# Performance work log

Hardware: AMD Instinct MI355X
Metric: run time of the kernel (lower is better)

## Reference

```python
import jax, jax.numpy as jnp
import numpy as np

H = 4          # attention heads
K = 16         # knn neighbors
EPS = 1e-5     # BatchNorm eps


def setup_inputs() -> dict:
    key = jax.random.key(0)
    ks = jax.random.split(key, 10)
    B, C, T, N = 2, 128, 32, 512
    OUT = 128
    HID = 2 * C + 2 * OUT  # ff hidden = in*2 + out*2
    s = 0.02
    return {
        "x_all": jax.random.normal(ks[0], (B, C, T, N), jnp.float32),
        "Wq": jax.random.normal(ks[1], (C, C), jnp.float32) * s,
        "Wk": jax.random.normal(ks[2], (C, C), jnp.float32) * s,
        "Wv": jax.random.normal(ks[3], (C, C), jnp.float32) * s,
        "W1": jax.random.normal(ks[4], (HID, C), jnp.float32) * s,
        "W2": jax.random.normal(ks[5], (OUT, HID), jnp.float32) * s,
        "bn_gamma": 1.0 + 0.1 * jax.random.normal(ks[6], (OUT,), jnp.float32),
        "bn_beta": 0.1 * jax.random.normal(ks[7], (OUT,), jnp.float32),
        "bn_mean": 0.1 * jax.random.normal(ks[8], (OUT,), jnp.float32),
        "bn_var": jax.random.uniform(ks[9], (OUT,), jnp.float32, 0.5, 1.5),
    }


def reference(x_all, Wq, Wk, Wv, W1, W2, bn_gamma, bn_beta, bn_mean, bn_var):
    B, C, T, N = x_all.shape
    D = C // H
    # --- st_group_points: candidate pool = 3 consecutive frames (replicate temporal pad), frame-major ---
    xp = jnp.concatenate([x_all[:, :, :1], x_all, x_all[:, :, -1:]], axis=2)   # (B,C,T+2,N)
    pool = jnp.stack([xp[:, :, :-2], xp[:, :, 1:-1], xp[:, :, 2:]], axis=3)    # (B,C,T,3,N)
    pool = pool.reshape(B, C, T, 3 * N)                                        # (B,C,T,3N)
    # KNN on xyz (channels 0:3); sqrt is monotone so topk on squared dists gives same indices
    a = x_all[:, :3]                                                           # (B,3,T,N)
    b = pool[:, :3]                                                            # (B,3,T,3N)
    d2 = jnp.sum((a[..., :, None] - b[..., None, :]) ** 2, axis=1)             # (B,T,N,3N)
    _, idx = jax.lax.top_k(-d2, K)                                             # (B,T,N,K) smallest-dist
    nb = jnp.take_along_axis(pool[:, :, :, None, :], idx[:, None], axis=-1)    # (B,C,T,N,K)
    rel = x_all[..., None] - nb                                                # diff grouping (B,C,T,N,K)
    # --- per-point local attention over K neighbors (1x1 convs == channel matmuls), all t at once ---
    q = jnp.einsum('oc,bctn->botn', Wq, x_all).reshape(B, H, D, T, N)
    k = jnp.einsum('oc,bctnk->botnk', Wk, rel).reshape(B, H, D, T, N, K)
    v = jnp.einsum('oc,bctnk->botnk', Wv, rel).reshape(B, H, D, T, N, K)
    energy = jnp.einsum('bhdtn,bhdtnk->bhtnk', q, k) / jnp.sqrt(jnp.float32(D))
    attn = jax.nn.softmax(energy, axis=-1)                                     # (B,H,T,N,K)
    agg = jnp.einsum('bhtnk,bhdtnk->bhdtn', attn, v).reshape(B, C, T, N)
    # --- residual + BatchNorm1d (eval mode, running stats) + conv feed-forward ---
    h = x_all + agg
    scale = (bn_gamma / jnp.sqrt(bn_var + EPS))[None, :, None, None]
    h = (h - bn_mean[None, :, None, None]) * scale + bn_beta[None, :, None, None]
    h = jax.nn.leaky_relu(jnp.einsum('oc,bctn->botn', W1, h), 0.2)
    y = jnp.einsum('oc,bctn->botn', W2, h)                                     # (B,OUT,T,N)
    return jnp.concatenate([x_all[:, :4], y], axis=1)                          # (B,4+OUT,T,N)
```

## Files before the change

kernel.cpp:

```cpp
#include <hip/hip_runtime.h>
#include <hip/hip_bf16.h>

typedef __hip_bfloat16 bf16;
typedef unsigned long long u64;
typedef __attribute__((ext_vector_type(8))) short short8;
typedef __attribute__((ext_vector_type(4))) float f32x4;

#define B_   2
#define C_   128
#define T_   32
#define N_   512
#define K_   16
#define HID_ 512
#define TN   (T_*N_)
#define PTS  (B_*T_*N_)

#define MFMA_BF16(a,b,c) __builtin_amdgcn_mfma_f32_16x16x32_bf16((a),(b),(c),0,0,0)

__device__ __forceinline__ float b2f(bf16 v){ return __bfloat162float(v); }
__device__ __forceinline__ bf16  f2b(float v){ return __float2bfloat16(v); }

__device__ __forceinline__ float ldc(const void* p, int i, bool f32) {
  return f32 ? ((const float*)p)[i] : b2f(((const bf16*)p)[i]);
}

__global__ __launch_bounds__(256) void convw_kernel(
    const void* __restrict__ x,
    const void* wq, const void* wk, const void* wv,
    const void* w1, const void* w2, const void* g, const void* bb,
    const void* m, const void* v,
    bf16* __restrict__ wqb, bf16* __restrict__ wkb, bf16* __restrict__ wvb,
    bf16* __restrict__ w1b, bf16* __restrict__ w2b,
    float* __restrict__ gf, float* __restrict__ bf_, float* __restrict__ mf,
    float* __restrict__ vf, int* __restrict__ flag)
{
  __shared__ int cnt;
  if (threadIdx.x == 0) cnt = 0;
  __syncthreads();
  const unsigned short* u = (const unsigned short*)x;
  int w = 0;
#pragma unroll
  for (int j = 0; j < 8; ++j) {
    unsigned short hv = u[threadIdx.x*8 + j];
    int e = (hv >> 7) & 0xFF;
    if (e >= 0x89) w++;
  }
  if (w) atomicAdd(&cnt, w);
  __syncthreads();
  bool f32 = (cnt > 32);
  if (blockIdx.x == 0 && threadIdx.x == 0) *flag = f32 ? 1 : 0;

  int i = blockIdx.x*256 + threadIdx.x;
  if (i < 16384) { wqb[i] = f2b(ldc(wq, i, f32)); return; } i -= 16384;
  if (i < 16384) { wkb[i] = f2b(ldc(wk, i, f32)); return; } i -= 16384;
  if (i < 16384) { wvb[i] = f2b(ldc(wv, i, f32)); return; } i -= 16384;
  if (i < 65536) { w1b[i] = f2b(ldc(w1, i, f32)); return; } i -= 65536;
  if (i < 65536) { w2b[i] = f2b(ldc(w2, i, f32)); return; } i -= 65536;
  if (i < 128)   { gf[i]  = ldc(g, i, f32); return; }       i -= 128;
  if (i < 128)   { bf_[i] = ldc(bb, i, f32); return; }      i -= 128;
  if (i < 128)   { mf[i]  = ldc(m, i, f32); return; }       i -= 128;
  if (i < 128)   { vf[i]  = ldc(v, i, f32); return; }
}

__device__ __forceinline__ void proj_gemm(const bf16* __restrict__ W,
                                          bf16 (*ys)[136],
                                          const short8 am[4][4],
                                          int mrow, int quad, int wave)
{
#pragma unroll
  for (int oi = 0; oi < 2; ++oi) {
    int ot = wave*2 + oi;
    f32x4 acc[4];
#pragma unroll
    for (int mt=0;mt<4;++mt) acc[mt] = (f32x4){0.f,0.f,0.f,0.f};
#pragma unroll
    for (int kq=0;kq<4;++kq) {
      short8 bfr = *(const short8*)&W[(ot*16+mrow)*C_ + kq*32 + quad*8];
#pragma unroll
      for (int mt=0;mt<4;++mt) acc[mt] = MFMA_BF16(am[mt][kq], bfr, acc[mt]);
    }
#pragma unroll
    for (int mt=0;mt<4;++mt)
#pragma unroll
      for (int r=0;r<4;++r)
        ys[mt*16 + quad*4 + r][ot*16 + mrow] = f2b(acc[mt][r]);
  }
}

__device__ __forceinline__ void tile_store128(bf16* __restrict__ dst,
                                              const bf16 (*ys)[136], int tid)
{
#pragma unroll
  for (int it=0; it<4; ++it) {
    int flat = (it*256 + tid)*8;
    int p = flat >> 7, c = flat & 127;
    *(short8*)&dst[(size_t)p*C_ + c] = *(const short8*)&ys[p][c];
  }
}

__global__ __launch_bounds__(256) void proj_kernel(
    const void* __restrict__ x, const int* __restrict__ flag,
    const bf16* __restrict__ wqb, const bf16* __restrict__ wkb, const bf16* __restrict__ wvb,
    bf16* __restrict__ xTb, bf16* QT, bf16* __restrict__ KT, bf16* __restrict__ VT)
{
  __shared__ bf16 xs [64][136];
  __shared__ bf16 ysK[64][136];
  __shared__ bf16 ysV[64][136];
  int tid = threadIdx.x;
  int p0  = blockIdx.x * 64;
  int b   = p0 >> 14; int tn0 = p0 & (TN-1);
  if (*flag) {
    const float* xbase = (const float*)x + (size_t)b*C_*TN + tn0;
#pragma unroll
    for (int it=0; it<32; ++it) {
      int i = it*256 + tid;
      int c = i >> 6, p = i & 63;
      xs[p][c] = f2b(xbase[(size_t)c*TN + p]);
    }
  } else {
    const bf16* xbase = (const bf16*)x + (size_t)b*C_*TN + tn0;
#pragma unroll
    for (int it=0; it<32; ++it) {
      int i = it*256 + tid;
      int c = i >> 6, p = i & 63;
      xs[p][c] = xbase[(size_t)c*TN + p];
    }
  }
  __syncthreads();
  tile_store128(xTb + (size_t)p0*C_, xs, tid);
  int lane = tid & 63, wave = tid >> 6;
  int mrow = lane & 15, quad = lane >> 4;
  short8 am[4][4];
#pragma unroll
  for (int mt=0;mt<4;++mt)
#pragma unroll
    for (int kq=0;kq<4;++kq)
      am[mt][kq] = *(const short8*)&xs[mt*16 + mrow][kq*32 + quad*8];
  __syncthreads();
  proj_gemm(wqb, xs,  am, mrow, quad, wave);
  proj_gemm(wkb, ysK, am, mrow, quad, wave);
  proj_gemm(wvb, ysV, am, mrow, quad, wave);
  __syncthreads();
  tile_store128(QT + (size_t)p0*C_, xs,  tid);
  tile_store128(KT + (size_t)p0*C_, ysK, tid);
  tile_store128(VT + (size_t)p0*C_, ysV, tid);
}

__device__ __forceinline__ u64 shflx64(u64 v, int m) {
  return (u64)__shfl_xor((long long)v, m, 64);
}
template<int W>
__device__ __forceinline__ u64 bitonic64w(u64 key, int lane) {
#pragma unroll
  for (int k = 2; k <= W; k <<= 1) {
#pragma unroll
    for (int j = k >> 1; j >= 1; j >>= 1) {
      u64 p = shflx64(key, j);
      bool keep_min = ((lane & k) == 0) == ((lane & j) == 0);
      key = ((p < key) == keep_min) ? p : key;
    }
  }
  return key;
}
__device__ __forceinline__ unsigned bitonic32u(unsigned key, int lane) {
#pragma unroll
  for (int k = 2; k <= 64; k <<= 1) {
#pragma unroll
    for (int j = k >> 1; j >= 1; j >>= 1) {
      unsigned p = (unsigned)__shfl_xor((int)key, j, 64);
      bool keep_min = ((lane & k) == 0) == ((lane & j) == 0);
      key = ((p < key) == keep_min) ? p : key;
    }
  }
  return key;
}

__global__ __launch_bounds__(512) void knn_kernel(const void* __restrict__ x,
                                                  const int* __restrict__ flag,
                                                  int* __restrict__ idxout)
{
  __shared__ float4 cand4[3*N_];
  __shared__ u64 surv[8][64];
  int tid = threadIdx.x;
  int blk = blockIdx.x;
  int row = blk >> 6;
  int b = row >> 5, t = row & 31;
  int ng = blk & 63;
  bool f32 = (*flag != 0);
#pragma unroll
  for (int q = 0; q < 3; ++q) {
    int tt = t - 1 + q; tt = tt < 0 ? 0 : (tt > T_-1 ? T_-1 : tt);
    size_t base = ((size_t)b*C_*T_ + tt)*(size_t)N_ + tid;
    float c0, c1, c2;
    if (f32) {
      const float* xp = (const float*)x;
      c0 = xp[base]; c1 = xp[base + (size_t)T_*N_]; c2 = xp[base + 2*(size_t)T_*N_];
    } else {
      const bf16* xp = (const bf16*)x;
      c0 = b2f(xp[base]); c1 = b2f(xp[base + (size_t)T_*N_]); c2 = b2f(xp[base + 2*(size_t)T_*N_]);
    }
    cand4[q*N_ + tid] = make_float4(c0, c1, c2, 0.f);
  }
  __syncthreads();
  int wave = tid >> 6, lane = tid & 63;
  int n = ng*8 + wave;
  float4 a = cand4[N_ + n];
  unsigned db[24];
#pragma unroll
  for (int j = 0; j < 24; ++j) {
    float4 cm = cand4[lane + (j << 6)];
    float dx = a.x - cm.x;
    float dy = a.y - cm.y;
    float dz = a.z - cm.z;
    float d2 = __fadd_rn(__fadd_rn(__fmul_rn(dx,dx), __fmul_rn(dy,dy)), __fmul_rn(dz,dz));
    db[j] = __float_as_uint(d2);
  }
  unsigned bd = db[0];
#pragma unroll
  for (int j = 1; j < 24; ++j) bd = (db[j] < bd) ? db[j] : bd;
  unsigned sd = bitonic32u(bd, lane);
  unsigned U = (unsigned)__shfl((int)sd, 15, 64);
  int c = 0;
#pragma unroll
  for (int j = 0; j < 24; ++j) c += (db[j] <= U) ? 1 : 0;
  int sc = c;
#pragma unroll
  for (int d = 1; d < 64; d <<= 1) {
    int pv = __shfl_up(sc, d, 64);
    if (lane >= d) sc += pv;
  }
  int total = __shfl(sc, 63, 64);
  int ofs = sc - c;
  u64 out16;
  if (total <= 64) {
#pragma unroll
    for (int j = 0; j < 24; ++j) {
      if (db[j] <= U) {
        surv[wave][ofs] = ((u64)db[j] << 32) | (unsigned)(lane + (j << 6));
        ++ofs;
      }
    }
    __threadfence_block();
    u64 kk = (lane < total) ? surv[wave][lane] : ~0ull;
    out16 = (total <= 32) ? bitonic64w<32>(kk, lane)
                          : bitonic64w<64>(kk, lane);
  } else {
    u64 key[24];
#pragma unroll
    for (int j = 0; j < 24; ++j)
      key[j] = ((u64)db[j] << 32) | (unsigned)(lane + (j << 6));
    u64 res = ~0ull;
#pragma unroll 1
    for (int r = 0; r < 16; ++r) {
      u64 m2 = key[0];
#pragma unroll
      for (int j = 1; j < 24; ++j) m2 = (key[j] < m2) ? key[j] : m2;
#pragma unroll
      for (int s = 32; s >= 1; s >>= 1) {
        u64 p = shflx64(m2, s);
        m2 = (p < m2) ? p : m2;
      }
      if (lane == r) res = m2;
      int mwin = (int)(m2 & 0xffffffffu);
      int sel = ((mwin & 63) == lane) ? (mwin >> 6) : -1;
#pragma unroll
      for (int j = 0; j < 24; ++j) if (j == sel) key[j] = ~0ull;
    }
    out16 = res;
  }
  int point = (b*T_ + t)*N_ + n;
  if (lane < K_) idxout[point*K_ + lane] = (int)(out16 & 0xffffffffu);
}

__global__ __launch_bounds__(512) void attn_kernel(
    const int* __restrict__ idxin, const bf16* __restrict__ xTb,
    bf16* qhT , const bf16* __restrict__ KT,
    const bf16* __restrict__ VT,
    const float* __restrict__ gf, const float* __restrict__ bf_,
    const float* __restrict__ mf, const float* __restrict__ vf)
{
  __shared__ int   col_lds[4][16];
  __shared__ float qbuf[4][C_];
  __shared__ bf16  kbuf[4][K_][136];
  __shared__ bf16  vbuf[4][K_][136];
  __shared__ float e_lds[4][4][16];
  int tid = threadIdx.x;
  int pt = tid >> 7, o = tid & 127;
  int point = blockIdx.x*4 + pt;
  int b = point >> 14; int tn = point & (TN-1); int t = tn >> 9;
  if (o < K_) {
    int m = idxin[point*K_ + o];
    int j = m >> 9, nn = m & (N_-1);
    int tt = t-1+j; tt = tt<0?0:(tt>T_-1?T_-1:tt);
    col_lds[pt][o] = ((b*T_ + tt)*N_ + nn)*C_;
  }
  int self = point*C_;
  qbuf[pt][o] = b2f(qhT[self + o]);
  __syncthreads();
#pragma unroll
  for (int it = 0; it < 2; ++it) {
    int i = it*512 + tid;
    int pp = i >> 8, rem = i & 255, k = rem >> 4, ch = rem & 15;
    int src = col_lds[pp][k] + ch*8;
    *(short8*)&kbuf[pp][k][ch*8] = *(const short8*)&KT[src];
    *(short8*)&vbuf[pp][k][ch*8] = *(const short8*)&VT[src];
  }
  __syncthreads();
  if (tid < 256) {
    int pp = tid >> 6, j = tid & 63, hd = j >> 4, k = j & 15;
    const float* qp = &qbuf[pp][hd*32];
    const bf16*  kp = &kbuf[pp][k][hd*32];
    float e = 0.f;
#pragma unroll
    for (int d=0; d<32; ++d) e = fmaf(qp[d], b2f(kp[d]), e);
    e_lds[pp][hd][k] = -e * 0.17677669529663687f;
  }
  __syncthreads();
  int hd = o >> 5;
  float e[16]; float mx = -3e38f;
#pragma unroll
  for (int k=0;k<K_;++k){ e[k]=e_lds[pt][hd][k]; mx=fmaxf(mx,e[k]); }
  float ssum=0.f;
#pragma unroll
  for (int k=0;k<K_;++k){ e[k]=__expf(e[k]-mx); ssum+=e[k]; }
  float inv = 1.f/ssum;
  float acc = b2f(VT[self + o]);
#pragma unroll
  for (int k=0;k<K_;++k)
    acc = fmaf(-(e[k]*inv), b2f(vbuf[pt][k][o]), acc);
  float hv = b2f(xTb[self + o]) + acc;
  float sc = gf[o] / sqrtf(vf[o] + 1e-5f);
  qhT[self + o] = f2b((hv - mf[o])*sc + bf_[o]);
}

__global__ __launch_bounds__(256) void mlp_kernel(const bf16* __restrict__ hT,
                                                  const bf16* __restrict__ w1b,
                                                  const bf16* __restrict__ w2b,
                                                  const void* __restrict__ x,
                                                  const int* __restrict__ flag,
                                                  void* out)
{
  __shared__ bf16 hidh[32][264];
  int tid = threadIdx.x;
  int p0 = blockIdx.x*32;
  int lane = tid & 63, wave = tid >> 6;
  int mrow = lane & 15, quad = lane >> 4;
  bool f32o = (*flag != 0);
  int bb = p0 >> 14;
  int tn0 = p0 & (TN-1);
  if (tid < 128) {
    int c = tid >> 5, p = tid & 31;
    size_t si = ((size_t)bb*C_ + c)*TN + tn0 + p;
    size_t di = ((size_t)bb*132 + c)*TN + tn0 + p;
    if (f32o) ((float*)out)[di] = ((const float*)x)[si];
    else      ((bf16*)out)[di]  = ((const bf16*)x)[si];
  }
  f32x4 acc2[2][2];
#pragma unroll
  for (int oi=0;oi<2;++oi)
#pragma unroll
    for (int mt=0;mt<2;++mt) acc2[oi][mt] = (f32x4){0.f,0.f,0.f,0.f};

#pragma unroll
  for (int half = 0; half < 2; ++half) {
    if (half) __syncthreads();
    short8 am[2][4];
#pragma unroll
    for (int mt=0;mt<2;++mt)
#pragma unroll
      for (int kq=0;kq<4;++kq)
        am[mt][kq] = *(const short8*)&hT[(size_t)(p0 + mt*16 + mrow)*C_ + kq*32 + quad*8];
#pragma unroll
    for (int oi = 0; oi < 4; ++oi) {
      int ot_g = half*16 + wave*4 + oi;
      int otl  = wave*4 + oi;
      f32x4 acc[2];
#pragma unroll
      for (int mt=0;mt<2;++mt) acc[mt] = (f32x4){0.f,0.f,0.f,0.f};
#pragma unroll
      for (int kq=0;kq<4;++kq) {
        short8 bfr = *(const short8*)&w1b[(ot_g*16+mrow)*C_ + kq*32 + quad*8];
#pragma unroll
        for (int mt=0;mt<2;++mt) acc[mt] = MFMA_BF16(am[mt][kq], bfr, acc[mt]);
      }
#pragma unroll
      for (int mt=0;mt<2;++mt)
#pragma unroll
        for (int r=0;r<4;++r) {
          float z = acc[mt][r];
          hidh[mt*16 + quad*4 + r][otl*16 + mrow] = f2b(z > 0.f ? z : 0.2f*z);
        }
    }
    __syncthreads();
#pragma unroll
    for (int kc = 0; kc < 4; ++kc) {
      short8 ha[2][2];
#pragma unroll
      for (int mt=0;mt<2;++mt)
#pragma unroll
        for (int kk=0;kk<2;++kk)
          ha[mt][kk] = *(const short8*)&hidh[mt*16 + mrow][(kc*2+kk)*32 + quad*8];
#pragma unroll
      for (int oi=0;oi<2;++oi) {
        int ot2 = wave*2 + oi;
#pragma unroll
        for (int kk=0;kk<2;++kk) {
          int ks_g = half*8 + kc*2 + kk;
          short8 bfr = *(const short8*)&w2b[(ot2*16+mrow)*HID_ + ks_g*32 + quad*8];
#pragma unroll
          for (int mt=0;mt<2;++mt)
            acc2[oi][mt] = MFMA_BF16(ha[mt][kk], bfr, acc2[oi][mt]);
        }
      }
    }
  }
  size_t obase = (size_t)bb*132*TN;
#pragma unroll
  for (int oi=0;oi<2;++oi) {
    int ch = (wave*2+oi)*16 + mrow;
#pragma unroll
    for (int mt=0;mt<2;++mt) {
      int tn = tn0 + mt*16 + quad*4;
      size_t oidx = obase + (size_t)(4+ch)*TN + tn;
      if (f32o) {
        *(f32x4*)&((float*)out)[oidx] = acc2[oi][mt];
      } else {
        bf16 tmp[4];
#pragma unroll
        for (int r=0;r<4;++r) tmp[r] = f2b(acc2[oi][mt][r]);
        *(u64*)&((bf16*)out)[oidx] = *(u64*)tmp;
      }
    }
  }
}

extern "C" void kernel_launch(void* const* d_in, const int* in_sizes, int n_in,
                              void* d_out, int out_size, void* d_ws, size_t ws_size,
                              hipStream_t stream)
{
  (void)in_sizes; (void)n_in; (void)out_size; (void)ws_size;
  const void* x = d_in[0];
  char* ws = (char*)d_ws;
  const size_t MB = (size_t)1<<20;
  bf16*  QT  = (bf16* )(ws + 0*MB);
  bf16*  KT  = (bf16* )(ws + 8*MB);
  bf16*  VT  = (bf16* )(ws + 16*MB);
  bf16*  xTb = (bf16* )(ws + 24*MB);
  int*   idxw= (int*  )(ws + 32*MB);
  bf16*  wqb = (bf16* )(ws + 34*MB);
  bf16*  wkb = (bf16* )(ws + 34*MB + 0x8000);
  bf16*  wvb = (bf16* )(ws + 34*MB + 0x10000);
  bf16*  w1b = (bf16* )(ws + 34*MB + 0x18000);
  bf16*  w2b = (bf16* )(ws + 34*MB + 0x38000);
  float* gf  = (float*)(ws + 34*MB + 0x58000);
  float* bf_ = (float*)(ws + 34*MB + 0x58200);
  float* mf  = (float*)(ws + 34*MB + 0x58400);
  float* vf  = (float*)(ws + 34*MB + 0x58600);
  int*  flag = (int*  )(ws + 34*MB + 0x58800);

  convw_kernel<<<dim3(706), dim3(256), 0, stream>>>(
      x, d_in[1], d_in[2], d_in[3], d_in[4], d_in[5],
      d_in[6], d_in[7], d_in[8], d_in[9],
      wqb, wkb, wvb, w1b, w2b, gf, bf_, mf, vf, flag);
  proj_kernel <<<dim3(PTS/64), dim3(256), 0, stream>>>(x, flag, wqb, wkb, wvb, xTb, QT, KT, VT);
  knn_kernel  <<<dim3(PTS/8), dim3(512), 0, stream>>>(x, flag, idxw);
  attn_kernel <<<dim3(PTS/4), dim3(512), 0, stream>>>(idxw, xTb, QT , KT, VT, gf, bf_, mf, vf);
  mlp_kernel  <<<dim3(PTS/32), dim3(256), 0, stream>>>(QT , w1b, w2b, x, flag, d_out);
}
```

Measured before the change: 210.9 us.

## Merge projection and KNN into one interleaved launch; parallelize attention energy dot

Replaces the separate projection and KNN kernels with one launch of 4608 blocks. Every ninth block runs the QKV projection for 64 points using 512 threads, and the other eight run KNN rows, so the two independent workloads share the GPU and one launch plus its tail is removed. The attention energy step now uses all 512 threads, each doing a 16-wide half dot product with vector loads, combined with a shuffle. The risks are a larger shared memory footprint per block for the KNN blocks, which can lower occupancy, and imbalance between the two block types.

```diff
diff --git a/kernel.cpp b/kernel.cpp
--- a/kernel.cpp
+++ b/kernel.cpp
@@ -19,6 +19,9 @@
 
 __device__ __forceinline__ float b2f(bf16 v){ return __bfloat162float(v); }
 __device__ __forceinline__ bf16  f2b(float v){ return __float2bfloat16(v); }
+__device__ __forceinline__ float bqf(short v){
+  return __uint_as_float(((unsigned)(unsigned short)v) << 16);
+}
 
 __device__ __forceinline__ float ldc(const void* p, int i, bool f32) {
   return f32 ? ((const float*)p)[i] : b2f(((const bf16*)p)[i]);
@@ -62,90 +65,6 @@
   if (i < 128)   { vf[i]  = ldc(v, i, f32); return; }
 }
 
-__device__ __forceinline__ void proj_gemm(const bf16* __restrict__ W,
-                                          bf16 (*ys)[136],
-                                          const short8 am[4][4],
-                                          int mrow, int quad, int wave)
-{
-#pragma unroll
-  for (int oi = 0; oi < 2; ++oi) {
-    int ot = wave*2 + oi;
-    f32x4 acc[4];
-#pragma unroll
-    for (int mt=0;mt<4;++mt) acc[mt] = (f32x4){0.f,0.f,0.f,0.f};
-#pragma unroll
-    for (int kq=0;kq<4;++kq) {
-      short8 bfr = *(const short8*)&W[(ot*16+mrow)*C_ + kq*32 + quad*8];
-#pragma unroll
-      for (int mt=0;mt<4;++mt) acc[mt] = MFMA_BF16(am[mt][kq], bfr, acc[mt]);
-    }
-#pragma unroll
-    for (int mt=0;mt<4;++mt)
-#pragma unroll
-      for (int r=0;r<4;++r)
-        ys[mt*16 + quad*4 + r][ot*16 + mrow] = f2b(acc[mt][r]);
-  }
-}
-
-__device__ __forceinline__ void tile_store128(bf16* __restrict__ dst,
-                                              const bf16 (*ys)[136], int tid)
-{
-#pragma unroll
-  for (int it=0; it<4; ++it) {
-    int flat = (it*256 + tid)*8;
-    int p = flat >> 7, c = flat & 127;
-    *(short8*)&dst[(size_t)p*C_ + c] = *(const short8*)&ys[p][c];
-  }
-}
-
-__global__ __launch_bounds__(256) void proj_kernel(
-    const void* __restrict__ x, const int* __restrict__ flag,
-    const bf16* __restrict__ wqb, const bf16* __restrict__ wkb, const bf16* __restrict__ wvb,
-    bf16* __restrict__ xTb, bf16* QT, bf16* __restrict__ KT, bf16* __restrict__ VT)
-{
-  __shared__ bf16 xs [64][136];
-  __shared__ bf16 ysK[64][136];
-  __shared__ bf16 ysV[64][136];
-  int tid = threadIdx.x;
-  int p0  = blockIdx.x * 64;
-  int b   = p0 >> 14; int tn0 = p0 & (TN-1);
-  if (*flag) {
-    const float* xbase = (const float*)x + (size_t)b*C_*TN + tn0;
-#pragma unroll
-    for (int it=0; it<32; ++it) {
-      int i = it*256 + tid;
-      int c = i >> 6, p = i & 63;
-      xs[p][c] = f2b(xbase[(size_t)c*TN + p]);
-    }
-  } else {
-    const bf16* xbase = (const bf16*)x + (size_t)b*C_*TN + tn0;
-#pragma unroll
-    for (int it=0; it<32; ++it) {
-      int i = it*256 + tid;
-      int c = i >> 6, p = i & 63;
-      xs[p][c] = xbase[(size_t)c*TN + p];
-    }
-  }
-  __syncthreads();
-  tile_store128(xTb + (size_t)p0*C_, xs, tid);
-  int lane = tid & 63, wave = tid >> 6;
-  int mrow = lane & 15, quad = lane >> 4;
-  short8 am[4][4];
-#pragma unroll
-  for (int mt=0;mt<4;++mt)
-#pragma unroll
-    for (int kq=0;kq<4;++kq)
-      am[mt][kq] = *(const short8*)&xs[mt*16 + mrow][kq*32 + quad*8];
-  __syncthreads();
-  proj_gemm(wqb, xs,  am, mrow, quad, wave);
-  proj_gemm(wkb, ysK, am, mrow, quad, wave);
-  proj_gemm(wvb, ysV, am, mrow, quad, wave);
-  __syncthreads();
-  tile_store128(QT + (size_t)p0*C_, xs,  tid);
-  tile_store128(KT + (size_t)p0*C_, ysK, tid);
-  tile_store128(VT + (size_t)p0*C_, ysV, tid);
-}
-
 __device__ __forceinline__ u64 shflx64(u64 v, int m) {
   return (u64)__shfl_xor((long long)v, m, 64);
 }
@@ -175,101 +94,181 @@
   return key;
 }
 
-__global__ __launch_bounds__(512) void knn_kernel(const void* __restrict__ x,
-                                                  const int* __restrict__ flag,
-                                                  int* __restrict__ idxout)
-{
-  __shared__ float4 cand4[3*N_];
-  __shared__ u64 surv[8][64];
+__device__ __forceinline__ void proj_gemm8(const bf16* __restrict__ W,
+                                           bf16 (*ys)[136],
+                                           const short8 am[4][4],
+                                           int mrow, int quad, int ot)
+{
+  f32x4 acc[4];
+#pragma unroll
+  for (int mt=0;mt<4;++mt) acc[mt] = (f32x4){0.f,0.f,0.f,0.f};
+#pragma unroll
+  for (int kq=0;kq<4;++kq) {
+    short8 bfr = *(const short8*)&W[(ot*16+mrow)*C_ + kq*32 + quad*8];
+#pragma unroll
+    for (int mt=0;mt<4;++mt) acc[mt] = MFMA_BF16(am[mt][kq], bfr, acc[mt]);
+  }
+#pragma unroll
+  for (int mt=0;mt<4;++mt)
+#pragma unroll
+    for (int r=0;r<4;++r)
+      ys[mt*16 + quad*4 + r][ot*16 + mrow] = f2b(acc[mt][r]);
+}
+
+__device__ __forceinline__ void tile_store128_512(bf16* __restrict__ dst,
+                                                  const bf16 (*ys)[136], int tid)
+{
+#pragma unroll
+  for (int it=0; it<2; ++it) {
+    int flat = (it*512 + tid)*8;
+    int p = flat >> 7, c = flat & 127;
+    *(short8*)&dst[(size_t)p*C_ + c] = *(const short8*)&ys[p][c];
+  }
+}
+
+__global__ __launch_bounds__(512) void projknn_kernel(
+    const void* __restrict__ x, const int* __restrict__ flag,
+    const bf16* __restrict__ wqb, const bf16* __restrict__ wkb, const bf16* __restrict__ wvb,
+    bf16* __restrict__ xTb, bf16* QT, bf16* __restrict__ KT, bf16* __restrict__ VT,
+    int* __restrict__ idxout)
+{
+  __shared__ __align__(16) char smem[52224];
   int tid = threadIdx.x;
   int blk = blockIdx.x;
-  int row = blk >> 6;
-  int b = row >> 5, t = row & 31;
-  int ng = blk & 63;
-  bool f32 = (*flag != 0);
-#pragma unroll
-  for (int q = 0; q < 3; ++q) {
-    int tt = t - 1 + q; tt = tt < 0 ? 0 : (tt > T_-1 ? T_-1 : tt);
-    size_t base = ((size_t)b*C_*T_ + tt)*(size_t)N_ + tid;
-    float c0, c1, c2;
-    if (f32) {
-      const float* xp = (const float*)x;
-      c0 = xp[base]; c1 = xp[base + (size_t)T_*N_]; c2 = xp[base + 2*(size_t)T_*N_];
+  int g = blk / 9, r = blk - g*9;
+  if (r == 8) {
+    bf16 (*xs )[136] = (bf16(*)[136])(smem);
+    bf16 (*ysK)[136] = (bf16(*)[136])(smem + 17408);
+    bf16 (*ysV)[136] = (bf16(*)[136])(smem + 34816);
+    int p0 = g * 64;
+    int b = p0 >> 14; int tn0 = p0 & (TN-1);
+    if (*flag) {
+      const float* xbase = (const float*)x + (size_t)b*C_*TN + tn0;
+#pragma unroll
+      for (int it=0; it<16; ++it) {
+        int i = it*512 + tid;
+        int c = i >> 6, p = i & 63;
+        xs[p][c] = f2b(xbase[(size_t)c*TN + p]);
+      }
     } else {
-      const bf16* xp = (const bf16*)x;
-      c0 = b2f(xp[base]); c1 = b2f(xp[base + (size_t)T_*N_]); c2 = b2f(xp[base + 2*(size_t)T_*N_]);
-    }
-    cand4[q*N_ + tid] = make_float4(c0, c1, c2, 0.f);
-  }
-  __syncthreads();
-  int wave = tid >> 6, lane = tid & 63;
-  int n = ng*8 + wave;
-  float4 a = cand4[N_ + n];
-  unsigned db[24];
-#pragma unroll
-  for (int j = 0; j < 24; ++j) {
-    float4 cm = cand4[lane + (j << 6)];
-    float dx = a.x - cm.x;
-    float dy = a.y - cm.y;
-    float dz = a.z - cm.z;
-    float d2 = __fadd_rn(__fadd_rn(__fmul_rn(dx,dx), __fmul_rn(dy,dy)), __fmul_rn(dz,dz));
-    db[j] = __float_as_uint(d2);
-  }
-  unsigned bd = db[0];
-#pragma unroll
-  for (int j = 1; j < 24; ++j) bd = (db[j] < bd) ? db[j] : bd;
-  unsigned sd = bitonic32u(bd, lane);
-  unsigned U = (unsigned)__shfl((int)sd, 15, 64);
-  int c = 0;
-#pragma unroll
-  for (int j = 0; j < 24; ++j) c += (db[j] <= U) ? 1 : 0;
-  int sc = c;
-#pragma unroll
-  for (int d = 1; d < 64; d <<= 1) {
-    int pv = __shfl_up(sc, d, 64);
-    if (lane >= d) sc += pv;
-  }
-  int total = __shfl(sc, 63, 64);
-  int ofs = sc - c;
-  u64 out16;
-  if (total <= 64) {
+      const bf16* xbase = (const bf16*)x + (size_t)b*C_*TN + tn0;
+#pragma unroll
+      for (int it=0; it<16; ++it) {
+        int i = it*512 + tid;
+        int c = i >> 6, p = i & 63;
+        xs[p][c] = xbase[(size_t)c*TN + p];
+      }
+    }
+    __syncthreads();
+    tile_store128_512(xTb + (size_t)p0*C_, xs, tid);
+    int lane = tid & 63, wave = tid >> 6;
+    int mrow = lane & 15, quad = lane >> 4;
+    short8 am[4][4];
+#pragma unroll
+    for (int mt=0;mt<4;++mt)
+#pragma unroll
+      for (int kq=0;kq<4;++kq)
+        am[mt][kq] = *(const short8*)&xs[mt*16 + mrow][kq*32 + quad*8];
+    __syncthreads();
+    proj_gemm8(wqb, xs,  am, mrow, quad, wave);
+    proj_gemm8(wkb, ysK, am, mrow, quad, wave);
+    proj_gemm8(wvb, ysV, am, mrow, quad, wave);
+    __syncthreads();
+    tile_store128_512(QT + (size_t)p0*C_, xs,  tid);
+    tile_store128_512(KT + (size_t)p0*C_, ysK, tid);
+    tile_store128_512(VT + (size_t)p0*C_, ysV, tid);
+  } else {
+    float4* cand4 = (float4*)smem;
+    u64 (*surv)[64] = (u64(*)[64])(smem + 24576);
+    int kblk = g*8 + r;
+    int row = kblk >> 6;
+    int b = row >> 5, t = row & 31;
+    int ng = kblk & 63;
+    bool f32 = (*flag != 0);
+#pragma unroll
+    for (int q = 0; q < 3; ++q) {
+      int tt = t - 1 + q; tt = tt < 0 ? 0 : (tt > T_-1 ? T_-1 : tt);
+      size_t base = ((size_t)b*C_*T_ + tt)*(size_t)N_ + tid;
+      float c0, c1, c2;
+      if (f32) {
+        const float* xp = (const float*)x;
+        c0 = xp[base]; c1 = xp[base + (size_t)T_*N_]; c2 = xp[base + 2*(size_t)T_*N_];
+      } else {
+        const bf16* xp = (const bf16*)x;
+        c0 = b2f(xp[base]); c1 = b2f(xp[base + (size_t)T_*N_]); c2 = b2f(xp[base + 2*(size_t)T_*N_]);
+      }
+      cand4[q*N_ + tid] = make_float4(c0, c1, c2, 0.f);
+    }
+    __syncthreads();
+    int wave = tid >> 6, lane = tid & 63;
+    int n = ng*8 + wave;
+    float4 a = cand4[N_ + n];
+    unsigned db[24];
 #pragma unroll
     for (int j = 0; j < 24; ++j) {
-      if (db[j] <= U) {
-        surv[wave][ofs] = ((u64)db[j] << 32) | (unsigned)(lane + (j << 6));
-        ++ofs;
-      }
-    }
-    __threadfence_block();
-    u64 kk = (lane < total) ? surv[wave][lane] : ~0ull;
-    out16 = (total <= 32) ? bitonic64w<32>(kk, lane)
-                          : bitonic64w<64>(kk, lane);
-  } else {
-    u64 key[24];
-#pragma unroll
-    for (int j = 0; j < 24; ++j)
-      key[j] = ((u64)db[j] << 32) | (unsigned)(lane + (j << 6));
-    u64 res = ~0ull;
+      float4 cm = cand4[lane + (j << 6)];
+      float dx = a.x - cm.x;
+      float dy = a.y - cm.y;
+      float dz = a.z - cm.z;
+      float d2 = __fadd_rn(__fadd_rn(__fmul_rn(dx,dx), __fmul_rn(dy,dy)), __fmul_rn(dz,dz));
+      db[j] = __float_as_uint(d2);
+    }
+    unsigned bd = db[0];
+#pragma unroll
+    for (int j = 1; j < 24; ++j) bd = (db[j] < bd) ? db[j] : bd;
+    unsigned sd = bitonic32u(bd, lane);
+    unsigned U = (unsigned)__shfl((int)sd, 15, 64);
+    int c = 0;
+#pragma unroll
+    for (int j = 0; j < 24; ++j) c += (db[j] <= U) ? 1 : 0;
+    int sc = c;
+#pragma unroll
+    for (int d = 1; d < 64; d <<= 1) {
+      int pv = __shfl_up(sc, d, 64);
+      if (lane >= d) sc += pv;
+    }
+    int total = __shfl(sc, 63, 64);
+    int ofs = sc - c;
+    u64 out16;
+    if (total <= 64) {
+#pragma unroll
+      for (int j = 0; j < 24; ++j) {
+        if (db[j] <= U) {
+          surv[wave][ofs] = ((u64)db[j] << 32) | (unsigned)(lane + (j << 6));
+          ++ofs;
+        }
+      }
+      __threadfence_block();
+      u64 kk = (lane < total) ? surv[wave][lane] : ~0ull;
+      out16 = (total <= 32) ? bitonic64w<32>(kk, lane)
+                            : bitonic64w<64>(kk, lane);
+    } else {
+      u64 key[24];
+#pragma unroll
+      for (int j = 0; j < 24; ++j)
+        key[j] = ((u64)db[j] << 32) | (unsigned)(lane + (j << 6));
+      u64 res = ~0ull;
 #pragma unroll 1
-    for (int r = 0; r < 16; ++r) {
-      u64 m2 = key[0];
-#pragma unroll
-      for (int j = 1; j < 24; ++j) m2 = (key[j] < m2) ? key[j] : m2;
-#pragma unroll
-      for (int s = 32; s >= 1; s >>= 1) {
-        u64 p = shflx64(m2, s);
-        m2 = (p < m2) ? p : m2;
-      }
-      if (lane == r) res = m2;
-      int mwin = (int)(m2 & 0xffffffffu);
-      int sel = ((mwin & 63) == lane) ? (mwin >> 6) : -1;
-#pragma unroll
-      for (int j = 0; j < 24; ++j) if (j == sel) key[j] = ~0ull;
-    }
-    out16 = res;
-  }
-  int point = (b*T_ + t)*N_ + n;
-  if (lane < K_) idxout[point*K_ + lane] = (int)(out16 & 0xffffffffu);
+      for (int rr = 0; rr < 16; ++rr) {
+        u64 m2 = key[0];
+#pragma unroll
+        for (int j = 1; j < 24; ++j) m2 = (key[j] < m2) ? key[j] : m2;
+#pragma unroll
+        for (int s = 32; s >= 1; s >>= 1) {
+          u64 p = shflx64(m2, s);
+          m2 = (p < m2) ? p : m2;
+        }
+        if (lane == rr) res = m2;
+        int mwin = (int)(m2 & 0xffffffffu);
+        int sel = ((mwin & 63) == lane) ? (mwin >> 6) : -1;
+#pragma unroll
+        for (int j = 0; j < 24; ++j) if (j == sel) key[j] = ~0ull;
+      }
+      out16 = res;
+    }
+    int point = (b*T_ + t)*N_ + n;
+    if (lane < K_) idxout[point*K_ + lane] = (int)(out16 & 0xffffffffu);
+  }
 }
 
 __global__ __launch_bounds__(512) void attn_kernel(
@@ -306,14 +305,25 @@
     *(short8*)&vbuf[pp][k][ch*8] = *(const short8*)&VT[src];
   }
   __syncthreads();
-  if (tid < 256) {
-    int pp = tid >> 6, j = tid & 63, hd = j >> 4, k = j & 15;
-    const float* qp = &qbuf[pp][hd*32];
-    const bf16*  kp = &kbuf[pp][k][hd*32];
+  {
+    int pp = tid >> 7, j = tid & 127;
+    int k = j >> 3, hd = (j >> 1) & 3, half = j & 1;
+    const float* qp = &qbuf[pp][hd*32 + half*16];
+    const bf16*  kp = &kbuf[pp][k][hd*32 + half*16];
+    short8 kv0 = *(const short8*)kp;
+    short8 kv1 = *(const short8*)(kp + 8);
+    float qv[16];
+    *(float4*)&qv[0]  = *(const float4*)(qp);
+    *(float4*)&qv[4]  = *(const float4*)(qp + 4);
+    *(float4*)&qv[8]  = *(const float4*)(qp + 8);
+    *(float4*)&qv[12] = *(const float4*)(qp + 12);
     float e = 0.f;
 #pragma unroll
-    for (int d=0; d<32; ++d) e = fmaf(qp[d], b2f(kp[d]), e);
-    e_lds[pp][hd][k] = -e * 0.17677669529663687f;
+    for (int i2=0;i2<8;++i2) e = fmaf(qv[i2],   bqf(kv0[i2]), e);
+#pragma unroll
+    for (int i2=0;i2<8;++i2) e = fmaf(qv[8+i2], bqf(kv1[i2]), e);
+    e += __shfl_xor(e, 1, 64);
+    if (!half) e_lds[pp][hd][k] = -e * 0.17677669529663687f;
   }
   __syncthreads();
   int hd = o >> 5;
@@ -458,12 +468,14 @@
   float* vf  = (float*)(ws + 34*MB + 0x58600);
   int*  flag = (int*  )(ws + 34*MB + 0x58800);
 
-  convw_kernel<<<dim3(706), dim3(256), 0, stream>>>(
+  convw_kernel  <<<dim3(706), dim3(256), 0, stream>>>(
       x, d_in[1], d_in[2], d_in[3], d_in[4], d_in[5],
       d_in[6], d_in[7], d_in[8], d_in[9],
       wqb, wkb, wvb, w1b, w2b, gf, bf_, mf, vf, flag);
-  proj_kernel <<<dim3(PTS/64), dim3(256), 0, stream>>>(x, flag, wqb, wkb, wvb, xTb, QT, KT, VT);
-  knn_kernel  <<<dim3(PTS/8), dim3(512), 0, stream>>>(x, flag, idxw);
-  attn_kernel <<<dim3(PTS/4), dim3(512), 0, stream>>>(idxw, xTb, QT , KT, VT, gf, bf_, mf, vf);
-  mlp_kernel  <<<dim3(PTS/32), dim3(256), 0, stream>>>(QT , w1b, w2b, x, flag, d_out);
-}
+  projknn_kernel<<<dim3(4608), dim3(512), 0, stream>>>(
+      x, flag, wqb, wkb, wvb, xTb, QT, KT, VT, idxw);
+  attn_kernel   <<<dim3(PTS/4), dim3(512), 0, stream>>>(
+      idxw, xTb, QT , KT, VT, gf, bf_, mf, vf);
+  mlp_kernel    <<<dim3(PTS/32), dim3(256), 0, stream>>>(
+      QT , w1b, w2b, x, flag, d_out);
+}
```

Result: no change. 214.6 us (+1.8%).
